# Performance work log

Hardware: AMD Instinct MI355X
Metric: run time of the kernel (lower is better)

Reference implementation:

```python
import jax, jax.numpy as jnp
import numpy as np

H = 1024          # hidden_size
NH = 16           # num_attention_heads
HD = H // NH      # head_dim = 64
FF = 4096         # intermediate_size
EPS = 1e-12       # layer_norm_eps
CLAMP = 1e9


def _layer_norm(x, gamma, beta):
    mu = jnp.mean(x, axis=-1, keepdims=True)
    var = jnp.mean(jnp.square(x - mu), axis=-1, keepdims=True)
    return (x - mu) * jax.lax.rsqrt(var + EPS) * gamma + beta


def setup_inputs() -> dict:
    key = jax.random.key(0)
    ks = jax.random.split(key, 12)
    B, S = 4, 2048
    s_h = 1.0 / np.sqrt(H)
    s_f = 1.0 / np.sqrt(FF)
    return {
        "hidden_states": jax.random.normal(ks[0], (B, S, H), jnp.float32),
        "Wq": jax.random.normal(ks[1], (H, H), jnp.float32) * s_h,
        "bq": jnp.zeros((H,), jnp.float32),
        "Wk": jax.random.normal(ks[2], (H, H), jnp.float32) * s_h,
        "bk": jnp.zeros((H,), jnp.float32),
        "Wv": jax.random.normal(ks[3], (H, H), jnp.float32) * s_h,
        "bv": jnp.zeros((H,), jnp.float32),
        "ln1_g": jnp.ones((H,), jnp.float32),
        "ln1_b": jnp.zeros((H,), jnp.float32),
        "W1": jax.random.normal(ks[4], (H, FF), jnp.float32) * s_h,
        "b1": jnp.zeros((FF,), jnp.float32),
        "W2": jax.random.normal(ks[5], (FF, H), jnp.float32) * s_f,
        "b2": jnp.zeros((H,), jnp.float32),
        "ln2_g": jnp.ones((H,), jnp.float32),
        "ln2_b": jnp.zeros((H,), jnp.float32),
    }


def reference(hidden_states, Wq, bq, Wk, bk, Wv, bv, ln1_g, ln1_b,
              W1, b1, W2, b2, ln2_g, ln2_b):
    B, S, _ = hidden_states.shape
    # QKV projections -> [B, NH, S, HD]
    def heads(x):
        return x.reshape(B, S, NH, HD).transpose(0, 2, 1, 3)
    q = heads(hidden_states @ Wq + bq)
    k = heads(hidden_states @ Wk + bk)
    v = heads(hidden_states @ Wv + bv)
    # manual attention: scale, clamp, softmax + 1e-9 epsilon
    scores = jnp.einsum('bhqd,bhkd->bhqk', q, k) / np.sqrt(HD)
    scores = jnp.clip(scores, -CLAMP, CLAMP)
    probs = jax.nn.softmax(scores, axis=-1) + 1e-9
    ctx = jnp.einsum('bhqk,bhkd->bhqd', probs, v)
    ctx = ctx.transpose(0, 2, 1, 3).reshape(B, S, NH * HD)
    # residual + LN (no output projection in this module)
    x = _layer_norm(hidden_states + ctx, ln1_g, ln1_b)
    # FFN with exact gelu + clamp
    inter = jax.nn.gelu(x @ W1 + b1, approximate=False)
    inter = jnp.clip(inter, -CLAMP, CLAMP)
    out = inter @ W2 + b2
    return _layer_norm(out + x, ln2_g, ln2_b)
```

## Files before the change

kernel.cpp:

```cpp
#include <hip/hip_runtime.h>
#include <math.h>


#define H_   1024
#define NH_  16
#define HD_  64
#define FF_  4096
#define S_   2048
#define B_   4
#define BS_  (B_ * S_)

#define EPI_NONE 0
#define EPI_GELU 1
#define EPI_QKV3 2

typedef unsigned short ushort_t;
typedef short v8s __attribute__((ext_vector_type(8)));
typedef float v4f __attribute__((ext_vector_type(4)));
typedef float v16f __attribute__((ext_vector_type(16)));

#define CQ_ 0.18033688011112042f

__device__ __forceinline__ unsigned short f2bf(float f) {
    union { float f; unsigned int u; } v; v.f = f;
    unsigned int u = v.u;
    return (unsigned short)((u + 0x7fffu + ((u >> 16) & 1u)) >> 16);
}
__device__ __forceinline__ float bf2f(unsigned short h) {
    union { unsigned int u; float f; } v; v.u = ((unsigned int)h) << 16;
    return v.f;
}

__device__ __forceinline__ unsigned cvt_pk_bf16(float lo, float hi) {
    unsigned r;
    asm("v_cvt_pk_bf16_f32 %0, %1, %2" : "=v"(r) : "v"(lo), "v"(hi));
    return r;
}
__device__ __forceinline__ void pl32_swap(unsigned &a, unsigned &b) {
    asm("v_permlane32_swap_b32 %0, %1" : "+v"(a), "+v"(b));
}

typedef __attribute__((address_space(1))) void gvoid;
typedef __attribute__((address_space(3))) void lvoid;
__device__ __forceinline__ void async16(const void* g, void* l) {
    __builtin_amdgcn_global_load_lds((gvoid*)g, (lvoid*)l, 16, 0, 0);
}

__global__ __launch_bounds__(256)
void cast_bf16_kernel(const float* __restrict__ x, ushort_t* __restrict__ y)
{
    const size_t i = ((size_t)blockIdx.x * 256 + threadIdx.x) * 4;
    float4 v = *(const float4*)&x[i];
    ushort4 o;
    o.x = f2bf(v.x); o.y = f2bf(v.y); o.z = f2bf(v.z); o.w = f2bf(v.w);
    *(ushort4*)&y[i] = o;
}

__global__ __launch_bounds__(256)
void cast_transpose_kernel(const float* __restrict__ W, ushort_t* __restrict__ Wt,
                           int K, int N)
{
    __shared__ float tile[32][33];
    const int tid = threadIdx.x;
    const int n0 = blockIdx.x * 32, k0 = blockIdx.y * 32;
    const int r  = tid >> 3;
    const int c4 = (tid & 7) * 4;
    float4 v = *(const float4*)&W[(size_t)(k0 + r) * N + n0 + c4];
    tile[r][c4 + 0] = v.x; tile[r][c4 + 1] = v.y;
    tile[r][c4 + 2] = v.z; tile[r][c4 + 3] = v.w;
    __syncthreads();
    ushort4 o;
    o.x = f2bf(tile[c4 + 0][r]); o.y = f2bf(tile[c4 + 1][r]);
    o.z = f2bf(tile[c4 + 2][r]); o.w = f2bf(tile[c4 + 3][r]);
    *(ushort4*)&Wt[(size_t)(n0 + r) * K + k0 + c4] = o;
}

__global__ __launch_bounds__(256)
void concat3_kernel(const float* __restrict__ a, const float* __restrict__ b,
                    const float* __restrict__ c, float* __restrict__ o)
{
    const int i = blockIdx.x * 256 + threadIdx.x;
    o[i] = (i < 1024) ? a[i] : (i < 2048) ? b[i - 1024] : c[i - 2048];
}

template <int EPI>
__global__ __launch_bounds__(256)
void bgemm_kernel(const ushort_t* __restrict__ A, const ushort_t* __restrict__ Bt,
                  const float* __restrict__ bias, void* __restrict__ Cout,
                  int M, int N, int K)
{
    __shared__ ushort_t Atile[3 * 128 * 32];
    __shared__ ushort_t Btile[3 * 128 * 32];

    const int tid  = threadIdx.x;
    const int wave = tid >> 6;
    const int lane = tid & 63;
    const int ml   = lane & 15;
    const int q8   = lane >> 4;
    const int wm   = wave >> 1, wn = wave & 1;
    const int blockM = blockIdx.y * 128;
    const int blockN = blockIdx.x * 128;

    v4f acc[4][4];
#pragma unroll
    for (int a = 0; a < 4; ++a)
#pragma unroll
        for (int b = 0; b < 4; ++b) acc[a][b] = (v4f)0.f;

    auto stage = [&](int buf, int ktile) {
        const int kt = ktile * 32;
#pragma unroll
        for (int i = 0; i < 2; ++i) {
            const int chunk = i * 256 + wave * 64 + lane;
            const int row = chunk >> 2;
            const int kp  = (chunk & 3) ^ (row & 3);
            async16(A  + (size_t)(blockM + row) * K + kt + kp * 8,
                    &Atile[buf * 4096 + chunk * 8]);
            async16(Bt + (size_t)(blockN + row) * K + kt + kp * 8,
                    &Btile[buf * 4096 + chunk * 8]);
        }
    };

    auto compute = [&](int buf) {
        v8s af[4], bfr[4];
#pragma unroll
        for (int a = 0; a < 4; ++a) {
            const int r = wm * 64 + a * 16 + ml;
            af[a] = *(const v8s*)&Atile[buf * 4096 + r * 32 + ((q8 ^ (r & 3)) * 8)];
        }
#pragma unroll
        for (int b = 0; b < 4; ++b) {
            const int r = wn * 64 + b * 16 + ml;
            bfr[b] = *(const v8s*)&Btile[buf * 4096 + r * 32 + ((q8 ^ (r & 3)) * 8)];
        }
        __builtin_amdgcn_s_setprio(1);
#pragma unroll
        for (int a = 0; a < 4; ++a)
#pragma unroll
            for (int b = 0; b < 4; ++b)
                acc[a][b] = __builtin_amdgcn_mfma_f32_16x16x32_bf16(
                    af[a], bfr[b], acc[a][b], 0, 0, 0);
        __builtin_amdgcn_s_setprio(0);
    };

    const int NT = K >> 5;

    stage(0, 0);
    stage(1, 1);
    asm volatile("s_waitcnt vmcnt(4)" ::: "memory");
    __builtin_amdgcn_s_barrier();
    __builtin_amdgcn_sched_barrier(0);

    int bc = 0, bs = 2;
    for (int t = 0; t < NT; ++t) {
        const bool more = (t + 2 < NT);
        if (more) {
            stage(bs, t + 2);
            bs = (bs == 2) ? 0 : bs + 1;
        }
        compute(bc);
        bc = (bc == 2) ? 0 : bc + 1;
        if (t < NT - 1) {
            asm volatile("s_waitcnt lgkmcnt(0)" ::: "memory");
            if (more) asm volatile("s_waitcnt vmcnt(4)" ::: "memory");
            else      asm volatile("s_waitcnt vmcnt(0)" ::: "memory");
            __builtin_amdgcn_s_barrier();
            __builtin_amdgcn_sched_barrier(0);
        }
    }

#pragma unroll
    for (int a = 0; a < 4; ++a) {
#pragma unroll
        for (int b = 0; b < 4; ++b) {
            const int n  = blockN + wn * 64 + b * 16 + ml;
            const float bn = bias[n];
            if (EPI == EPI_QKV3) {
                const int nn = n & 1023;
                const int hh = nn >> 6, dd = nn & 63;
                ushort_t* base = (ushort_t*)Cout + (size_t)(n >> 10) * ((size_t)BS_ * H_);
                if (n < 2048) {
                    const float sc = (n < 1024) ? CQ_ : 1.f;
#pragma unroll
                    for (int r = 0; r < 4; ++r) {
                        const int m = blockM + wm * 64 + a * 16 + q8 * 4 + r;
                        base[(((size_t)((m >> 11) * NH_ + hh)) * S_ + (m & 2047)) * HD_ + dd]
                            = f2bf((acc[a][b][r] + bn) * sc);
                    }
                } else {
                    const int m0 = blockM + wm * 64 + a * 16 + q8 * 4;
                    ushort4 pk;
                    pk.x = f2bf(acc[a][b][0] + bn);
                    pk.y = f2bf(acc[a][b][1] + bn);
                    pk.z = f2bf(acc[a][b][2] + bn);
                    pk.w = f2bf(acc[a][b][3] + bn);
                    *(ushort4*)&base[(((size_t)((m0 >> 11) * NH_ + hh)) * HD_ + dd) * S_
                                     + (m0 & 2047)] = pk;
                }
            } else {
#pragma unroll
                for (int r = 0; r < 4; ++r) {
                    const int m = blockM + wm * 64 + a * 16 + q8 * 4 + r;
                    float v = acc[a][b][r] + bn;
                    if (EPI == EPI_GELU) {
                        v = v * 0.5f * (1.f + erff(v * 0.70710678118654752f));
                        v = fminf(fmaxf(v, -1e9f), 1e9f);
                        ((ushort_t*)Cout)[(size_t)m * N + n] = f2bf(v);
                    } else {
                        ((float*)Cout)[(size_t)m * N + n] = v;
                    }
                }
            }
        }
    }
}

__global__ __launch_bounds__(256)
void vsum_kernel(const ushort_t* __restrict__ VT, float* __restrict__ vsum)
{
    const int bh   = blockIdx.x;
    const int tid  = threadIdx.x;
    const int d    = tid >> 2;
    const int part = tid & 3;
    const ushort_t* p = VT + (size_t)bh * HD_ * S_ + (size_t)d * S_ + part * 512;
    float acc = 0.f;
    for (int i = 0; i < 512; i += 4) {
        ushort4 u = *(const ushort4*)&p[i];
        acc += (bf2f(u.x) + bf2f(u.y)) + (bf2f(u.z) + bf2f(u.w));
    }
    acc += __shfl_xor(acc, 1);
    acc += __shfl_xor(acc, 2);
    if (part == 0) vsum[bh * HD_ + d] = acc;
}

__global__ __launch_bounds__(256, 4)
void flash_kernel(const ushort_t* __restrict__ Q, const ushort_t* __restrict__ Kg,
                  const ushort_t* __restrict__ VT, const float* __restrict__ vsum,
                  float* __restrict__ ctx)
{
    __shared__ ushort_t Qs[128 * 64];
    __shared__ ushort_t Ks[64 * 64];
    __shared__ ushort_t Vs[64 * 64];

    int wg = blockIdx.x;
    wg = (wg & 7) * 128 + (wg >> 3);
    const int bh = wg >> 4;
    const int q0 = (wg & 15) * 128;

    const int tid  = threadIdx.x;
    const int wave = tid >> 6;
    const int lane = tid & 63;
    const int m    = lane & 31;
    const int hi   = lane >> 5;

    const ushort_t* Qp = Q  + (size_t)bh * S_ * HD_ + (size_t)q0 * HD_;
    const ushort_t* Kp = Kg + (size_t)bh * S_ * HD_;
    const ushort_t* Vp = VT + (size_t)bh * HD_ * S_;

#pragma unroll
    for (int i = 0; i < 4; ++i) {
        const int ch = i * 256 + tid;
        const int row = ch >> 3, c = ch & 7;
        async16(Qp + (size_t)row * HD_ + ((c ^ (row & 7)) * 8), &Qs[ch * 8]);
    }

    v16f o0 = (v16f)0.f, o1 = (v16f)0.f;
    float lp0 = 0.f, lp1 = 0.f, lp2 = 0.f, lp3 = 0.f;
    v8s qf[4];
    v8s pf[4];

    for (int t = 0; t < S_ / 64; ++t) {
        const int kv0 = t * 64;
        __syncthreads();
#pragma unroll
        for (int i = 0; i < 2; ++i) {
            const int ch = i * 256 + tid;
            const int row = ch >> 3, c = ch & 7;
            async16(Kp + (size_t)(kv0 + row) * HD_ + ((c ^ (row & 7)) * 8),
                    &Ks[ch * 8]);
            async16(Vp + (size_t)row * S_ + kv0 + ((c ^ (row & 7)) * 8),
                    &Vs[ch * 8]);
        }
        __syncthreads();

        if (t == 0) {
            const int qrow = wave * 32 + m;
#pragma unroll
            for (int c = 0; c < 4; ++c)
                qf[c] = *(const v8s*)&Qs[qrow * 64 + (((2 * c + hi) ^ (qrow & 7)) * 8)];
        }

#pragma unroll
        for (int a = 0; a < 2; ++a) {
            v16f z = (v16f)0.f;
            const int krow = a * 32 + m;
#pragma unroll
            for (int c = 0; c < 4; ++c) {
                v8s kf = *(const v8s*)&Ks[krow * 64 + (((2 * c + hi) ^ (m & 7)) * 8)];
                z = __builtin_amdgcn_mfma_f32_32x32x16_bf16(kf, qf[c], z, 0, 0, 0);
            }
            unsigned u[8];
#pragma unroll
            for (int mm = 0; mm < 8; ++mm) {
                const float plo = __builtin_exp2f(z[2 * mm]);
                const float phi = __builtin_exp2f(z[2 * mm + 1]);
                if ((mm & 3) == 0)      lp0 += plo + phi;
                else if ((mm & 3) == 1) lp1 += plo + phi;
                else if ((mm & 3) == 2) lp2 += plo + phi;
                else                    lp3 += plo + phi;
                u[mm] = cvt_pk_bf16(plo, phi);
            }
            pl32_swap(u[0], u[2]); pl32_swap(u[1], u[3]);
            pl32_swap(u[4], u[6]); pl32_swap(u[5], u[7]);
            union { unsigned w[4]; v8s s; } c0, c1;
            c0.w[0] = u[0]; c0.w[1] = u[1]; c0.w[2] = u[2]; c0.w[3] = u[3];
            c1.w[0] = u[4]; c1.w[1] = u[5]; c1.w[2] = u[6]; c1.w[3] = u[7];
            pf[2 * a]     = c0.s;
            pf[2 * a + 1] = c1.s;
        }

#pragma unroll
        for (int c = 0; c < 4; ++c) {
            const int sw = ((2 * c + hi) ^ (m & 7)) * 8;
            v8s vf0 = *(const v8s*)&Vs[m * 64 + sw];
            v8s vf1 = *(const v8s*)&Vs[(32 + m) * 64 + sw];
            o0 = __builtin_amdgcn_mfma_f32_32x32x16_bf16(vf0, pf[c], o0, 0, 0, 0);
            o1 = __builtin_amdgcn_mfma_f32_32x32x16_bf16(vf1, pf[c], o1, 0, 0, 0);
        }
    }

    float l_r = (lp0 + lp1) + (lp2 + lp3);
    l_r += __shfl_xor(l_r, 32);
    const float linv = 1.f / l_r;

    const int bb = bh >> 4, hh = bh & 15;
    const int srow = q0 + wave * 32 + m;
    float* cp = ctx + ((size_t)(bb * S_ + srow)) * H_ + hh * HD_;
#pragma unroll
    for (int g = 0; g < 2; ++g) {
        const v16f& o = g ? o1 : o0;
#pragma unroll
        for (int rq = 0; rq < 4; ++rq) {
            const int d0 = g * 32 + rq * 8 + hi * 4;
            float4 vs4 = *(const float4*)&vsum[bh * HD_ + d0];
            float4 ov;
            ov.x = o[rq * 4 + 0] * linv + 1e-9f * vs4.x;
            ov.y = o[rq * 4 + 1] * linv + 1e-9f * vs4.y;
            ov.z = o[rq * 4 + 2] * linv + 1e-9f * vs4.z;
            ov.w = o[rq * 4 + 3] * linv + 1e-9f * vs4.w;
            *(float4*)&cp[d0] = ov;
        }
    }
}

template <bool WB>
__global__ __launch_bounds__(256)
void add_ln_kernel(const float* __restrict__ A, const float* __restrict__ Bv,
                   const float* __restrict__ gamma, const float* __restrict__ beta,
                   float* __restrict__ out, ushort_t* __restrict__ outb)
{
    const int row = blockIdx.x;
    const int tid = threadIdx.x;
    const float* a = A  + (size_t)row * H_;
    const float* b = Bv + (size_t)row * H_;

    float4 av = *(const float4*)&a[tid * 4];
    float4 bv = *(const float4*)&b[tid * 4];
    float x[4] = { av.x + bv.x, av.y + bv.y, av.z + bv.z, av.w + bv.w };

    float s  = x[0] + x[1] + x[2] + x[3];
    float s2 = x[0]*x[0] + x[1]*x[1] + x[2]*x[2] + x[3]*x[3];
#pragma unroll
    for (int off = 1; off < 64; off <<= 1) {
        s  += __shfl_xor(s,  off);
        s2 += __shfl_xor(s2, off);
    }
    __shared__ float rs[8];
    const int wave = tid >> 6, lane = tid & 63;
    if (lane == 0) { rs[wave] = s; rs[4 + wave] = s2; }
    __syncthreads();
    const float sum  = rs[0] + rs[1] + rs[2] + rs[3];
    const float sum2 = rs[4] + rs[5] + rs[6] + rs[7];
    const float mu   = sum * (1.f / H_);
    const float var  = sum2 * (1.f / H_) - mu * mu;
    const float rstd = rsqrtf(var + 1e-12f);

    float4 gv = *(const float4*)&gamma[tid * 4];
    float4 be = *(const float4*)&beta[tid * 4];
    float4 ov;
    ov.x = (x[0] - mu) * rstd * gv.x + be.x;
    ov.y = (x[1] - mu) * rstd * gv.y + be.y;
    ov.z = (x[2] - mu) * rstd * gv.z + be.z;
    ov.w = (x[3] - mu) * rstd * gv.w + be.w;
    *(float4*)&out[(size_t)row * H_ + tid * 4] = ov;
    if (WB) {
        ushort4 ob;
        ob.x = f2bf(ov.x); ob.y = f2bf(ov.y); ob.z = f2bf(ov.z); ob.w = f2bf(ov.w);
        *(ushort4*)&outb[(size_t)row * H_ + tid * 4] = ob;
    }
}

extern "C" void kernel_launch(void* const* d_in, const int* in_sizes, int n_in,
                              void* d_out, int out_size, void* d_ws, size_t ws_size,
                              hipStream_t stream)
{
    const float* hidden = (const float*)d_in[0];
    const float* Wq     = (const float*)d_in[1];
    const float* bq     = (const float*)d_in[2];
    const float* Wk     = (const float*)d_in[3];
    const float* bk     = (const float*)d_in[4];
    const float* Wv     = (const float*)d_in[5];
    const float* bv     = (const float*)d_in[6];
    const float* ln1_g  = (const float*)d_in[7];
    const float* ln1_b  = (const float*)d_in[8];
    const float* W1     = (const float*)d_in[9];
    const float* b1     = (const float*)d_in[10];
    const float* W2     = (const float*)d_in[11];
    const float* b2     = (const float*)d_in[12];
    const float* ln2_g  = (const float*)d_in[13];
    const float* ln2_b  = (const float*)d_in[14];

    char* ws = (char*)d_ws;
    const size_t MB = 1024 * 1024;
    ushort_t* Xb    = (ushort_t*)(ws + 0);
    ushort_t* x1b   = (ushort_t*)(ws + 0);
    ushort_t* Wqt   = (ushort_t*)(ws + 16 * MB);
    ushort_t* Wkt   = (ushort_t*)(ws + 18 * MB);
    ushort_t* Wvt   = (ushort_t*)(ws + 20 * MB);
    ushort_t* W1t   = (ushort_t*)(ws + 16 * MB);
    ushort_t* W2t   = (ushort_t*)(ws + 24 * MB);
    ushort_t* q     = (ushort_t*)(ws + 32 * MB);
    ushort_t* k     = (ushort_t*)(ws + 48 * MB);
    ushort_t* vt    = (ushort_t*)(ws + 64 * MB);
    float*    ctx   = (float*)(ws + 80 * MB);
    ushort_t* inter = (ushort_t*)(ws + 32 * MB);
    float*    bcat  = (float*)(ws + 96 * MB);
    float*    vsum  = (float*)(ws + 96 * MB + 16384);
    float*    out2  = (float*)(ws + 96 * MB);
    float*    x1    = (float*)(ws + 128 * MB);
    float*    out   = (float*)d_out;

    const dim3 blk(256);

    cast_bf16_kernel<<<dim3(BS_ * H_ / 1024), blk, 0, stream>>>(hidden, Xb);
    cast_transpose_kernel<<<dim3(32, 32),  blk, 0, stream>>>(Wq, Wqt, H_, H_);
    cast_transpose_kernel<<<dim3(32, 32),  blk, 0, stream>>>(Wk, Wkt, H_, H_);
    cast_transpose_kernel<<<dim3(32, 32),  blk, 0, stream>>>(Wv, Wvt, H_, H_);
    cast_transpose_kernel<<<dim3(32, 128), blk, 0, stream>>>(W2, W2t, FF_, H_);
    concat3_kernel<<<dim3(12), blk, 0, stream>>>(bq, bk, bv, bcat);

    bgemm_kernel<EPI_QKV3><<<dim3(24, 64), blk, 0, stream>>>(
        Xb, Wqt, bcat, q, BS_, 3 * H_, H_);

    cast_transpose_kernel<<<dim3(128, 32), blk, 0, stream>>>(W1, W1t, H_, FF_);

    vsum_kernel<<<dim3(B_ * NH_), blk, 0, stream>>>(vt, vsum);

    flash_kernel<<<dim3((S_ / 128) * (B_ * NH_)), blk, 0, stream>>>(q, k, vt, vsum, ctx);

    add_ln_kernel<true><<<dim3(BS_), blk, 0, stream>>>(hidden, ctx, ln1_g, ln1_b, x1, x1b);

    bgemm_kernel<EPI_GELU><<<dim3(32, 64), blk, 0, stream>>>(x1b, W1t, b1, inter, BS_, FF_, H_);

    bgemm_kernel<EPI_NONE><<<dim3(8, 64), blk, 0, stream>>>(inter, W2t, b2, out2, BS_, H_, FF_);

    add_ln_kernel<false><<<dim3(BS_), blk, 0, stream>>>(out2, x1, ln2_g, ln2_b, out, nullptr);
}
```

Baseline: 605.2 us.

## Switch GEMM to 32x32x16 MFMA with 4-stage pipeline and XCD-aware tile remap

```diff
diff --git a/kernel.cpp b/kernel.cpp
--- a/kernel.cpp
+++ b/kernel.cpp
@@ -89,57 +89,63 @@
                   const float* __restrict__ bias, void* __restrict__ Cout,
                   int M, int N, int K)
 {
-    __shared__ ushort_t Atile[3 * 128 * 32];
-    __shared__ ushort_t Btile[3 * 128 * 32];
+    __shared__ ushort_t Atile[4 * 128 * 32];
+    __shared__ ushort_t Btile[4 * 128 * 32];
 
     const int tid  = threadIdx.x;
     const int wave = tid >> 6;
     const int lane = tid & 63;
-    const int ml   = lane & 15;
-    const int q8   = lane >> 4;
+    const int m    = lane & 31;
+    const int hi   = lane >> 5;
     const int wm   = wave >> 1, wn = wave & 1;
-    const int blockM = blockIdx.y * 128;
-    const int blockN = blockIdx.x * 128;
-
-    v4f acc[4][4];
-#pragma unroll
-    for (int a = 0; a < 4; ++a)
-#pragma unroll
-        for (int b = 0; b < 4; ++b) acc[a][b] = (v4f)0.f;
+
+    const int nper = (gridDim.x * gridDim.y) >> 3;
+    const int lid  = blockIdx.x + gridDim.x * blockIdx.y;
+    const int r_   = (lid & 7) * nper + (lid >> 3);
+    const int blockM = (r_ & 63) * 128;
+    const int blockN = (r_ >> 6) * 128;
+
+    v16f acc[2][2];
+#pragma unroll
+    for (int a = 0; a < 2; ++a)
+#pragma unroll
+        for (int b = 0; b < 2; ++b) acc[a][b] = (v16f)0.f;
 
     auto stage = [&](int buf, int ktile) {
         const int kt = ktile * 32;
 #pragma unroll
         for (int i = 0; i < 2; ++i) {
-            const int chunk = i * 256 + wave * 64 + lane;
+            const int chunk = i * 256 + tid;
             const int row = chunk >> 2;
-            const int kp  = (chunk & 3) ^ (row & 3);
-            async16(A  + (size_t)(blockM + row) * K + kt + kp * 8,
+            const int g   = (chunk & 3) ^ ((row >> 1) & 3);
+            async16(A  + (size_t)(blockM + row) * K + kt + g * 8,
                     &Atile[buf * 4096 + chunk * 8]);
-            async16(Bt + (size_t)(blockN + row) * K + kt + kp * 8,
+            async16(Bt + (size_t)(blockN + row) * K + kt + g * 8,
                     &Btile[buf * 4096 + chunk * 8]);
         }
     };
 
+    const int sw = (m >> 1) & 3;
     auto compute = [&](int buf) {
-        v8s af[4], bfr[4];
-#pragma unroll
-        for (int a = 0; a < 4; ++a) {
-            const int r = wm * 64 + a * 16 + ml;
-            af[a] = *(const v8s*)&Atile[buf * 4096 + r * 32 + ((q8 ^ (r & 3)) * 8)];
-        }
-#pragma unroll
-        for (int b = 0; b < 4; ++b) {
-            const int r = wn * 64 + b * 16 + ml;
-            bfr[b] = *(const v8s*)&Btile[buf * 4096 + r * 32 + ((q8 ^ (r & 3)) * 8)];
+        v8s af[2][2], bfr[2][2];
+#pragma unroll
+        for (int w = 0; w < 2; ++w) {
+            const int slot = (((w * 2 + hi) ^ sw)) * 8;
+#pragma unroll
+            for (int f = 0; f < 2; ++f) {
+                af[w][f]  = *(const v8s*)&Atile[buf * 4096 + (wm * 64 + f * 32 + m) * 32 + slot];
+                bfr[w][f] = *(const v8s*)&Btile[buf * 4096 + (wn * 64 + f * 32 + m) * 32 + slot];
+            }
         }
         __builtin_amdgcn_s_setprio(1);
 #pragma unroll
-        for (int a = 0; a < 4; ++a)
-#pragma unroll
-            for (int b = 0; b < 4; ++b)
-                acc[a][b] = __builtin_amdgcn_mfma_f32_16x16x32_bf16(
-                    af[a], bfr[b], acc[a][b], 0, 0, 0);
+        for (int w = 0; w < 2; ++w)
+#pragma unroll
+            for (int a = 0; a < 2; ++a)
+#pragma unroll
+                for (int b = 0; b < 2; ++b)
+                    acc[a][b] = __builtin_amdgcn_mfma_f32_32x32x16_bf16(
+                        af[w][a], bfr[w][b], acc[a][b], 0, 0, 0);
         __builtin_amdgcn_s_setprio(0);
     };
 
@@ -147,33 +153,29 @@
 
     stage(0, 0);
     stage(1, 1);
-    asm volatile("s_waitcnt vmcnt(4)" ::: "memory");
+    stage(2, 2);
+    asm volatile("s_waitcnt vmcnt(8)" ::: "memory");
     __builtin_amdgcn_s_barrier();
     __builtin_amdgcn_sched_barrier(0);
 
-    int bc = 0, bs = 2;
     for (int t = 0; t < NT; ++t) {
-        const bool more = (t + 2 < NT);
-        if (more) {
-            stage(bs, t + 2);
-            bs = (bs == 2) ? 0 : bs + 1;
-        }
-        compute(bc);
-        bc = (bc == 2) ? 0 : bc + 1;
+        if (t + 3 < NT) stage((t + 3) & 3, t + 3);
+        compute(t & 3);
         if (t < NT - 1) {
             asm volatile("s_waitcnt lgkmcnt(0)" ::: "memory");
-            if (more) asm volatile("s_waitcnt vmcnt(4)" ::: "memory");
-            else      asm volatile("s_waitcnt vmcnt(0)" ::: "memory");
+            if (t + 3 < NT)      asm volatile("s_waitcnt vmcnt(8)" ::: "memory");
+            else if (t + 2 < NT) asm volatile("s_waitcnt vmcnt(4)" ::: "memory");
+            else                 asm volatile("s_waitcnt vmcnt(0)" ::: "memory");
             __builtin_amdgcn_s_barrier();
             __builtin_amdgcn_sched_barrier(0);
         }
     }
 
 #pragma unroll
-    for (int a = 0; a < 4; ++a) {
-#pragma unroll
-        for (int b = 0; b < 4; ++b) {
-            const int n  = blockN + wn * 64 + b * 16 + ml;
+    for (int im = 0; im < 2; ++im) {
+#pragma unroll
+        for (int in = 0; in < 2; ++in) {
+            const int n  = blockN + wn * 64 + in * 32 + m;
             const float bn = bias[n];
             if (EPI == EPI_QKV3) {
                 const int nn = n & 1023;
@@ -182,34 +184,41 @@
                 if (n < 2048) {
                     const float sc = (n < 1024) ? CQ_ : 1.f;
 #pragma unroll
-                    for (int r = 0; r < 4; ++r) {
-                        const int m = blockM + wm * 64 + a * 16 + q8 * 4 + r;
-                        base[(((size_t)((m >> 11) * NH_ + hh)) * S_ + (m & 2047)) * HD_ + dd]
-                            = f2bf((acc[a][b][r] + bn) * sc);
+                    for (int g = 0; g < 4; ++g)
+#pragma unroll
+                        for (int rr = 0; rr < 4; ++rr) {
+                            const int mr = blockM + wm * 64 + im * 32 + g * 8 + hi * 4 + rr;
+                            base[(((size_t)((mr >> 11) * NH_ + hh)) * S_ + (mr & 2047)) * HD_ + dd]
+                                = f2bf((acc[im][in][g * 4 + rr] + bn) * sc);
+                        }
+                } else {
+#pragma unroll
+                    for (int g = 0; g < 4; ++g) {
+                        const int m0 = blockM + wm * 64 + im * 32 + g * 8 + hi * 4;
+                        ushort4 pk;
+                        pk.x = f2bf(acc[im][in][g * 4 + 0] + bn);
+                        pk.y = f2bf(acc[im][in][g * 4 + 1] + bn);
+                        pk.z = f2bf(acc[im][in][g * 4 + 2] + bn);
+                        pk.w = f2bf(acc[im][in][g * 4 + 3] + bn);
+                        *(ushort4*)&base[(((size_t)((m0 >> 11) * NH_ + hh)) * HD_ + dd) * S_
+                                         + (m0 & 2047)] = pk;
                     }
-                } else {
-                    const int m0 = blockM + wm * 64 + a * 16 + q8 * 4;
-                    ushort4 pk;
-                    pk.x = f2bf(acc[a][b][0] + bn);
-                    pk.y = f2bf(acc[a][b][1] + bn);
-                    pk.z = f2bf(acc[a][b][2] + bn);
-                    pk.w = f2bf(acc[a][b][3] + bn);
-                    *(ushort4*)&base[(((size_t)((m0 >> 11) * NH_ + hh)) * HD_ + dd) * S_
-                                     + (m0 & 2047)] = pk;
                 }
             } else {
 #pragma unroll
-                for (int r = 0; r < 4; ++r) {
-                    const int m = blockM + wm * 64 + a * 16 + q8 * 4 + r;
-                    float v = acc[a][b][r] + bn;
-                    if (EPI == EPI_GELU) {
-                        v = v * 0.5f * (1.f + erff(v * 0.70710678118654752f));
-                        v = fminf(fmaxf(v, -1e9f), 1e9f);
-                        ((ushort_t*)Cout)[(size_t)m * N + n] = f2bf(v);
-                    } else {
-                        ((float*)Cout)[(size_t)m * N + n] = v;
+                for (int g = 0; g < 4; ++g)
+#pragma unroll
+                    for (int rr = 0; rr < 4; ++rr) {
+                        const int mr = blockM + wm * 64 + im * 32 + g * 8 + hi * 4 + rr;
+                        float v = acc[im][in][g * 4 + rr] + bn;
+                        if (EPI == EPI_GELU) {
+                            v = v * 0.5f * (1.f + erff(v * 0.70710678118654752f));
+                            v = fminf(fmaxf(v, -1e9f), 1e9f);
+                            ((ushort_t*)Cout)[(size_t)mr * N + n] = f2bf(v);
+                        } else {
+                            ((float*)Cout)[(size_t)mr * N + n] = v;
+                        }
                     }
-                }
             }
         }
     }
```

After: 650.9 us. +7.6%, slower.
